# Kernel optimization log

Measured on AMD Instinct MI355X. Metric: run time of the kernel, lower is better.

## Reference

```python
import jax, jax.numpy as jnp
import numpy as np
import math

B, LC, LQ, D = 64, 1024, 128, 128


def setup_inputs() -> dict:
    key = jax.random.key(0)
    k1, k2, k3, k4, k5 = jax.random.split(key, 5)
    c_rep = jax.random.normal(k1, (B, LC, D), dtype=jnp.float32)
    q_rep = jax.random.normal(k2, (B, LQ, D), dtype=jnp.float32)
    c_mask = jax.random.randint(k3, (B, LC), 0, 2, dtype=jnp.int32)
    q_mask = jax.random.randint(k4, (B, LQ), 0, 2, dtype=jnp.int32)
    lim = math.sqrt(1.0 / D)
    w = jax.random.uniform(k5, (3 * D,), dtype=jnp.float32, minval=-lim, maxval=lim)
    return {"c_rep": c_rep, "q_rep": q_rep, "c_mask": c_mask, "q_mask": q_mask, "w": w}


def _mask_logits(t, m):
    # mask == 1 means masked (matches original: target*(1-mask) + mask*-1e30)
    return t * (1.0 - m) + m * (-1e30)


def reference(c_rep, q_rep, c_mask, q_mask, w):
    d = c_rep.shape[-1]
    w1, w2, w3 = w[:d], w[d:2 * d], w[2 * d:]
    # Trilinear similarity S[b,i,j] = <ct,w1> + <qt,w2> + <ct*qt,w3>
    # computed without materializing the [B,Lc,Lq,3D] concat tensor.
    S = (c_rep @ w1)[:, :, None] \
        + (q_rep @ w2)[:, None, :] \
        + jnp.einsum('bid,bjd->bij', c_rep * w3, q_rep)  # [B, Lc, Lq]
    qm = q_mask[:, None, :].astype(S.dtype)  # [B, 1, Lq]
    cm = c_mask[:, :, None].astype(S.dtype)  # [B, Lc, 1]
    S1 = jax.nn.softmax(_mask_logits(S, qm), axis=2)  # softmax over query dim
    S2 = jax.nn.softmax(_mask_logits(S, cm), axis=1)  # softmax over context dim
    A = jnp.einsum('bij,bjd->bid', S1, q_rep)  # [B, Lc, D]
    # B_att = S1 @ S2^T @ c_rep, associated right-first to avoid [B,Lc,Lc]
    T = jnp.einsum('bkj,bkd->bjd', S2, c_rep)  # [B, Lq, D]
    B_att = jnp.einsum('bij,bjd->bid', S1, T)  # [B, Lc, D]
    out = jnp.concatenate([c_rep, A, c_rep * A, c_rep * B_att], axis=2)  # [B, Lc, 4D]
    # dropout is identity at inference
    return out
```

## Files before the change

### kernel.cpp

```cpp
#include <hip/hip_runtime.h>
#include <hip/hip_bf16.h>
#include <cstdint>
#include <cstddef>

#define B_   64
#define LC_  1024
#define LQ_  128
#define D_   128

typedef __bf16 bf16;
typedef bf16  bf16x8 __attribute__((ext_vector_type(8)));
typedef bf16  bf16x4 __attribute__((ext_vector_type(4)));
typedef float f32x4  __attribute__((ext_vector_type(4)));

__device__ __forceinline__ f32x4 mfma16(bf16x8 a, bf16x8 b, f32x4 c) {
  return __builtin_amdgcn_mfma_f32_16x16x32_bf16(a, b, c, 0, 0, 0);
}

__global__ __launch_bounds__(256) void k0c(const float* __restrict__ c, const float* __restrict__ w,
                                           float* __restrict__ cw1, bf16* __restrict__ cw3,
                                           bf16* __restrict__ cT) {
  __shared__ float w1s[128];
  __shared__ float w3s[128];
  __shared__ bf16  ctile[128 * 132];
  const int b = blockIdx.y, ks = blockIdx.x;
  const int k0 = ks * 128;
  const int t = threadIdx.x;
  if (t < 128) { w1s[t] = w[t]; w3s[t] = w[256 + t]; }
  __syncthreads();
  {
    const int r = t >> 1, d0 = (t & 1) * 64;
    const float* crow = c + ((size_t)(b * LC_ + k0 + r) * D_ + d0);
    bf16* orow = cw3 + ((size_t)(b * LC_ + k0 + r) * D_ + d0);
    float dot = 0.f;
#pragma unroll
    for (int v = 0; v < 8; ++v) {
      const float4 f0 = ((const float4*)crow)[v * 2 + 0];
      const float4 f1 = ((const float4*)crow)[v * 2 + 1];
      const int dd = d0 + v * 8;
      dot += f0.x * w1s[dd + 0] + f0.y * w1s[dd + 1] + f0.z * w1s[dd + 2] + f0.w * w1s[dd + 3]
           + f1.x * w1s[dd + 4] + f1.y * w1s[dd + 5] + f1.z * w1s[dd + 6] + f1.w * w1s[dd + 7];
      bf16* cr = &ctile[r * 132 + dd];
      cr[0] = (bf16)f0.x; cr[1] = (bf16)f0.y; cr[2] = (bf16)f0.z; cr[3] = (bf16)f0.w;
      cr[4] = (bf16)f1.x; cr[5] = (bf16)f1.y; cr[6] = (bf16)f1.z; cr[7] = (bf16)f1.w;
      bf16x8 o;
      o[0] = (bf16)(f0.x * w3s[dd + 0]); o[1] = (bf16)(f0.y * w3s[dd + 1]);
      o[2] = (bf16)(f0.z * w3s[dd + 2]); o[3] = (bf16)(f0.w * w3s[dd + 3]);
      o[4] = (bf16)(f1.x * w3s[dd + 4]); o[5] = (bf16)(f1.y * w3s[dd + 5]);
      o[6] = (bf16)(f1.z * w3s[dd + 6]); o[7] = (bf16)(f1.w * w3s[dd + 7]);
      *(bf16x8*)(orow + v * 8) = o;
    }
    dot += __shfl_xor(dot, 1);
    if ((t & 1) == 0) cw1[b * LC_ + k0 + r] = dot;
  }
  __syncthreads();
  {
    const int d = t >> 1, kh = (t & 1) * 64;
    bf16* trow = cT + ((size_t)(b * D_ + d) * LC_ + k0 + kh);
#pragma unroll
    for (int v = 0; v < 8; ++v) {
      bf16x8 o;
#pragma unroll
      for (int e = 0; e < 8; ++e) o[e] = ctile[(kh + v * 8 + e) * 132 + d];
      *(bf16x8*)(trow + v * 8) = o;
    }
  }
}

__global__ __launch_bounds__(256) void k0q(const float* __restrict__ q, const float* __restrict__ w,
                                           float* __restrict__ qw2, bf16* __restrict__ qb,
                                           bf16* __restrict__ qT) {
  __shared__ float w2s[128];
  __shared__ bf16  qtile[128 * 132];
  const int b = blockIdx.x;
  const int t = threadIdx.x;
  if (t < 128) w2s[t] = w[128 + t];
  __syncthreads();
  {
    const int r = t >> 1, d0 = (t & 1) * 64;
    const float* qrow = q + ((size_t)(b * LQ_ + r) * D_ + d0);
    bf16* orow = qb + ((size_t)(b * LQ_ + r) * D_ + d0);
    float dot = 0.f;
#pragma unroll
    for (int v = 0; v < 8; ++v) {
      const float4 f0 = ((const float4*)qrow)[v * 2 + 0];
      const float4 f1 = ((const float4*)qrow)[v * 2 + 1];
      const int dd = d0 + v * 8;
      dot += f0.x * w2s[dd + 0] + f0.y * w2s[dd + 1] + f0.z * w2s[dd + 2] + f0.w * w2s[dd + 3]
           + f1.x * w2s[dd + 4] + f1.y * w2s[dd + 5] + f1.z * w2s[dd + 6] + f1.w * w2s[dd + 7];
      bf16x8 o;
      o[0] = (bf16)f0.x; o[1] = (bf16)f0.y; o[2] = (bf16)f0.z; o[3] = (bf16)f0.w;
      o[4] = (bf16)f1.x; o[5] = (bf16)f1.y; o[6] = (bf16)f1.z; o[7] = (bf16)f1.w;
      bf16* qr = &qtile[r * 132 + dd];
#pragma unroll
      for (int e = 0; e < 8; ++e) qr[e] = o[e];
      *(bf16x8*)(orow + v * 8) = o;
    }
    dot += __shfl_xor(dot, 1);
    if ((t & 1) == 0) qw2[b * LQ_ + r] = dot;
  }
  __syncthreads();
  {
    const int d = t >> 1, jh = (t & 1) * 64;
    bf16* trow = qT + ((size_t)(b * D_ + d) * LQ_ + jh);
#pragma unroll
    for (int v = 0; v < 8; ++v) {
      bf16x8 o;
#pragma unroll
      for (int e = 0; e < 8; ++e) o[e] = qtile[(jh + v * 8 + e) * 132 + d];
      *(bf16x8*)(trow + v * 8) = o;
    }
  }
}

__global__ __launch_bounds__(256) void k1(const float* __restrict__ cw1, const float* __restrict__ qw2,
                                          const int* __restrict__ cmask,
                                          const bf16* __restrict__ cw3, const bf16* __restrict__ cT,
                                          const bf16* __restrict__ qb, bf16* __restrict__ TT) {
  __shared__ bf16  qs[32 * 136];
  __shared__ bf16  cw3t[64 * 136];
  __shared__ bf16  cTt[128 * 72];
  __shared__ bf16  PT[32 * 72];
  __shared__ float lred[4][32];
  __shared__ float lfin[32];
  const int js = blockIdx.x, b = blockIdx.y;
  const int j0 = js * 32;
  const int t = threadIdx.x;
  const int w = t >> 6, lane = t & 63, quad = lane >> 4, l15 = lane & 15;

#pragma unroll
  for (int idx = t; idx < 512; idx += 256) {
    const int row = idx >> 4, ch = idx & 15;
    *(bf16x8*)&qs[row * 136 + ch * 8] =
        *(const bf16x8*)(qb + ((size_t)(b * LQ_ + j0 + row) * D_ + ch * 8));
  }
  const f32x4 z = {0.f, 0.f, 0.f, 0.f};
  f32x4 Tacc[2][2] = {{z, z}, {z, z}};
  float lacc0 = 0.f, lacc1 = 0.f;
  __syncthreads();

  for (int kt = 0; kt < 16; ++kt) {
    const int k0g = kt * 64;
#pragma unroll
    for (int idx = t; idx < 1024; idx += 256) {
      const int row = idx >> 4, ch = idx & 15;
      *(bf16x8*)&cw3t[row * 136 + ch * 8] =
          *(const bf16x8*)(cw3 + ((size_t)(b * LC_ + k0g + row) * D_ + ch * 8));
    }
#pragma unroll
    for (int idx = t; idx < 1024; idx += 256) {
      const int row = idx >> 3, ch = idx & 7;
      *(bf16x8*)&cTt[row * 72 + ch * 8] =
          *(const bf16x8*)(cT + ((size_t)(b * D_ + row) * LC_ + k0g + ch * 8));
    }
    __syncthreads();

    f32x4 S0 = z, S1 = z;
#pragma unroll
    for (int ks = 0; ks < 4; ++ks) {
      bf16x8 a  = *(bf16x8*)&cw3t[(w * 16 + l15) * 136 + ks * 32 + quad * 8];
      bf16x8 b0 = *(bf16x8*)&qs[l15 * 136 + ks * 32 + quad * 8];
      bf16x8 b1 = *(bf16x8*)&qs[(16 + l15) * 136 + ks * 32 + quad * 8];
      S0 = mfma16(a, b0, S0);
      S1 = mfma16(a, b1, S1);
    }
    const float qv0 = qw2[b * LQ_ + j0 + l15];
    const float qv1 = qw2[b * LQ_ + j0 + 16 + l15];
    bf16x4 pk0, pk1;
#pragma unroll
    for (int rr = 0; rr < 4; ++rr) {
      const int krow = k0g + w * 16 + quad * 4 + rr;
      const float c1 = cw1[b * LC_ + krow];
      const int   cm = cmask[b * LC_ + krow];
      const float p0 = cm ? 0.f : __expf(S0[rr] + c1 + qv0);
      const float p1 = cm ? 0.f : __expf(S1[rr] + c1 + qv1);
      lacc0 += p0; lacc1 += p1;
      pk0[rr] = (bf16)p0; pk1[rr] = (bf16)p1;
    }
    *(bf16x4*)&PT[l15 * 72 + w * 16 + quad * 4] = pk0;
    *(bf16x4*)&PT[(16 + l15) * 72 + w * 16 + quad * 4] = pk1;
    __syncthreads();

#pragma unroll
    for (int ks = 0; ks < 2; ++ks) {
      bf16x8 a0 = *(bf16x8*)&PT[l15 * 72 + ks * 32 + quad * 8];
      bf16x8 a1 = *(bf16x8*)&PT[(16 + l15) * 72 + ks * 32 + quad * 8];
      bf16x8 b0 = *(bf16x8*)&cTt[(w * 32 + l15) * 72 + ks * 32 + quad * 8];
      bf16x8 b1 = *(bf16x8*)&cTt[(w * 32 + 16 + l15) * 72 + ks * 32 + quad * 8];
      Tacc[0][0] = mfma16(a0, b0, Tacc[0][0]);
      Tacc[0][1] = mfma16(a0, b1, Tacc[0][1]);
      Tacc[1][0] = mfma16(a1, b0, Tacc[1][0]);
      Tacc[1][1] = mfma16(a1, b1, Tacc[1][1]);
    }
    __syncthreads();
  }

  lacc0 += __shfl_xor(lacc0, 16); lacc0 += __shfl_xor(lacc0, 32);
  lacc1 += __shfl_xor(lacc1, 16); lacc1 += __shfl_xor(lacc1, 32);
  if (lane < 16) { lred[w][l15] = lacc0; lred[w][16 + l15] = lacc1; }
  __syncthreads();
  if (t < 32) lfin[t] = lred[0][t] + lred[1][t] + lred[2][t] + lred[3][t];
  __syncthreads();

  bf16* TTa = cw3t;
#pragma unroll
  for (int mt = 0; mt < 2; ++mt) {
#pragma unroll
    for (int nt = 0; nt < 2; ++nt) {
      const int d = w * 32 + nt * 16 + l15;
      bf16x4 pk;
#pragma unroll
      for (int rr = 0; rr < 4; ++rr) {
        const int j = mt * 16 + quad * 4 + rr;
        pk[rr] = (bf16)(Tacc[mt][nt][rr] / lfin[j]);
      }
      *(bf16x4*)&TTa[d * 40 + mt * 16 + quad * 4] = pk;
    }
  }
  __syncthreads();
  if (t < 128) {
    bf16* dst = TT + ((size_t)(b * D_ + t) * LQ_ + j0);
#pragma unroll
    for (int v = 0; v < 4; ++v)
      *(bf16x8*)(dst + v * 8) = *(bf16x8*)&TTa[t * 40 + v * 8];
  }
}

__global__ __launch_bounds__(256) void k2(const float* __restrict__ c, const float* __restrict__ cw1,
                                          const float* __restrict__ qw2, const int* __restrict__ qmask,
                                          const bf16* __restrict__ cw3, const bf16* __restrict__ qb,
                                          const bf16* __restrict__ qT, const bf16* __restrict__ TT,
                                          float* __restrict__ out) {
  __shared__ bf16 cw3i[64 * 136];
  __shared__ bf16 qsl[32 * 136];
  __shared__ bf16 qTsl[128 * 40];
  __shared__ bf16 TTsl[128 * 40];
  __shared__ bf16 P1[64 * 40];
  const int it = blockIdx.x, b = blockIdx.y;
  const int i0 = it * 64;
  const int t = threadIdx.x;
  const int w = t >> 6, lane = t & 63, quad = lane >> 4, l15 = lane & 15;

#pragma unroll
  for (int idx = t; idx < 1024; idx += 256) {
    const int row = idx >> 4, ch = idx & 15;
    *(bf16x8*)&cw3i[row * 136 + ch * 8] =
        *(const bf16x8*)(cw3 + ((size_t)(b * LC_ + i0 + row) * D_ + ch * 8));
  }
  const f32x4 z = {0.f, 0.f, 0.f, 0.f};
  f32x4 Aacc[8], Bacc[8];
#pragma unroll
  for (int n = 0; n < 8; ++n) { Aacc[n] = z; Bacc[n] = z; }
  float lacc[4] = {0.f, 0.f, 0.f, 0.f};
  __syncthreads();

  for (int jt = 0; jt < 4; ++jt) {
    const int j0 = jt * 32;
#pragma unroll
    for (int idx = t; idx < 512; idx += 256) {
      const int row = idx >> 4, ch = idx & 15;
      *(bf16x8*)&qsl[row * 136 + ch * 8] =
          *(const bf16x8*)(qb + ((size_t)(b * LQ_ + j0 + row) * D_ + ch * 8));
    }
#pragma unroll
    for (int idx = t; idx < 512; idx += 256) {
      const int row = idx >> 2, ch = idx & 3;
      *(bf16x8*)&qTsl[row * 40 + ch * 8] =
          *(const bf16x8*)(qT + ((size_t)(b * D_ + row) * LQ_ + j0 + ch * 8));
    }
#pragma unroll
    for (int idx = t; idx < 512; idx += 256) {
      const int row = idx >> 2, ch = idx & 3;
      *(bf16x8*)&TTsl[row * 40 + ch * 8] =
          *(const bf16x8*)(TT + ((size_t)(b * D_ + row) * LQ_ + j0 + ch * 8));
    }
    __syncthreads();

    f32x4 S0 = z, S1 = z;
#pragma unroll
    for (int ks = 0; ks < 4; ++ks) {
      bf16x8 a  = *(bf16x8*)&cw3i[(w * 16 + l15) * 136 + ks * 32 + quad * 8];
      bf16x8 b0 = *(bf16x8*)&qsl[l15 * 136 + ks * 32 + quad * 8];
      bf16x8 b1 = *(bf16x8*)&qsl[(16 + l15) * 136 + ks * 32 + quad * 8];
      S0 = mfma16(a, b0, S0);
      S1 = mfma16(a, b1, S1);
    }
    const float qv0 = qw2[b * LQ_ + j0 + l15];
    const float qv1 = qw2[b * LQ_ + j0 + 16 + l15];
    const int   qm0 = qmask[b * LQ_ + j0 + l15];
    const int   qm1 = qmask[b * LQ_ + j0 + 16 + l15];
#pragma unroll
    for (int rr = 0; rr < 4; ++rr) {
      const int irow = i0 + w * 16 + quad * 4 + rr;
      const float c1 = cw1[b * LC_ + irow];
      const float p0 = qm0 ? 0.f : __expf(S0[rr] + c1 + qv0);
      const float p1 = qm1 ? 0.f : __expf(S1[rr] + c1 + qv1);
      lacc[rr] += p0 + p1;
      P1[(w * 16 + quad * 4 + rr) * 40 + l15] = (bf16)p0;
      P1[(w * 16 + quad * 4 + rr) * 40 + 16 + l15] = (bf16)p1;
    }
    __syncthreads();

    bf16x8 aP = *(bf16x8*)&P1[(w * 16 + l15) * 40 + quad * 8];
#pragma unroll
    for (int nt = 0; nt < 8; ++nt) {
      bf16x8 bq = *(bf16x8*)&qTsl[(nt * 16 + l15) * 40 + quad * 8];
      bf16x8 bt = *(bf16x8*)&TTsl[(nt * 16 + l15) * 40 + quad * 8];
      Aacc[nt] = mfma16(aP, bq, Aacc[nt]);
      Bacc[nt] = mfma16(aP, bt, Bacc[nt]);
    }
    __syncthreads();
  }

#pragma unroll
  for (int rr = 0; rr < 4; ++rr) {
    float v = lacc[rr];
    v += __shfl_xor(v, 1); v += __shfl_xor(v, 2);
    v += __shfl_xor(v, 4); v += __shfl_xor(v, 8);
    lacc[rr] = 1.f / v;
  }

#pragma unroll
  for (int nt = 0; nt < 8; ++nt) {
    const int d = nt * 16 + l15;
#pragma unroll
    for (int rr = 0; rr < 4; ++rr) {
      const int irow = i0 + w * 16 + quad * 4 + rr;
      const float Av = Aacc[nt][rr] * lacc[rr];
      const float Bv = Bacc[nt][rr] * lacc[rr];
      const float cv = c[(size_t)(b * LC_ + irow) * D_ + d];
      float* ob = out + (size_t)(b * LC_ + irow) * 512;
      ob[128 + d] = Av;
      ob[256 + d] = cv * Av;
      ob[384 + d] = cv * Bv;
    }
  }
#pragma unroll
  for (int idx = t; idx < 2048; idx += 256) {
    const int row = idx >> 5, seg = idx & 31;
    const float4 v = ((const float4*)(c + (size_t)(b * LC_ + i0 + row) * D_))[seg];
    ((float4*)(out + (size_t)(b * LC_ + i0 + row) * 512))[seg] = v;
  }
}

extern "C" void kernel_launch(void* const* d_in, const int* in_sizes, int n_in,
                              void* d_out, int out_size, void* d_ws, size_t ws_size,
                              hipStream_t stream) {
  (void)in_sizes; (void)n_in; (void)out_size; (void)ws_size;
  const float* c     = (const float*)d_in[0];
  const float* q     = (const float*)d_in[1];
  const int*   cmask = (const int*)d_in[2];
  const int*   qmask = (const int*)d_in[3];
  const float* w     = (const float*)d_in[4];
  float* out = (float*)d_out;

  char* ws = (char*)d_ws;
  float* cw1 = (float*)(ws + 0);
  float* qw2 = (float*)(ws + 262144);
  bf16*  cw3 = (bf16*)(ws + 294912);
  bf16*  cT  = (bf16*)(ws + 17072128);
  bf16*  qb  = (bf16*)(ws + 33849344);
  bf16*  qT  = (bf16*)(ws + 35946496);
  bf16*  TT  = (bf16*)(ws + 38043648);

  k0c<<<dim3(8, 64), 256, 0, stream>>>(c, w, cw1, cw3, cT);
  k0q<<<dim3(64), 256, 0, stream>>>(q, w, qw2, qb, qT);
  k1<<<dim3(4, 64), 256, 0, stream>>>(cw1, qw2, cmask, cw3, cT, qb, TT);
  k2<<<dim3(16, 64), 256, 0, stream>>>(c, cw1, qw2, qmask, cw3, qb, qT, TT, out);
}
```

Before: 266.0 us.

## Split k1 context reduction across blocks and stage k2 output through LDS

The k1 context-dimension reduction is split into two halves computed by separate blocks, doubling the grid from 256 to 512 blocks. Partial T sums and softmax denominators are written as fp32 into the output buffer as scratch, then combined and normalised by a new reduction kernel k1r. Separately, k2 now stages the A and B accumulators through shared memory so the output write becomes coalesced float4 stores of all four concatenated segments. This adds a kernel launch and extra fp32 partial traffic, and k2 gains extra syncs, in exchange for better occupancy in k1 and wider, coalesced stores in k2.

Result: faster. 246.8 us (-7.2%).

```diff
diff --git a/kernel.cpp b/kernel.cpp
--- a/kernel.cpp
+++ b/kernel.cpp
@@ -113,17 +113,19 @@
   }
 }
 
-__global__ __launch_bounds__(256) void k1(const float* __restrict__ cw1, const float* __restrict__ qw2,
-                                          const int* __restrict__ cmask,
-                                          const bf16* __restrict__ cw3, const bf16* __restrict__ cT,
-                                          const bf16* __restrict__ qb, bf16* __restrict__ TT) {
+__global__ __launch_bounds__(256) void k1p(const float* __restrict__ cw1, const float* __restrict__ qw2,
+                                           const int* __restrict__ cmask,
+                                           const bf16* __restrict__ cw3, const bf16* __restrict__ cT,
+                                           const bf16* __restrict__ qb,
+                                           float* __restrict__ Tpart, float* __restrict__ lpart) {
   __shared__ bf16  qs[32 * 136];
   __shared__ bf16  cw3t[64 * 136];
   __shared__ bf16  cTt[128 * 72];
   __shared__ bf16  PT[32 * 72];
   __shared__ float lred[4][32];
-  __shared__ float lfin[32];
-  const int js = blockIdx.x, b = blockIdx.y;
+  const int bx = blockIdx.x;
+  const int ks = bx >> 2, js = bx & 3;
+  const int b = blockIdx.y;
   const int j0 = js * 32;
   const int t = threadIdx.x;
   const int w = t >> 6, lane = t & 63, quad = lane >> 4, l15 = lane & 15;
@@ -139,8 +141,8 @@
   float lacc0 = 0.f, lacc1 = 0.f;
   __syncthreads();
 
-  for (int kt = 0; kt < 16; ++kt) {
-    const int k0g = kt * 64;
+  for (int kt = 0; kt < 8; ++kt) {
+    const int k0g = ks * 512 + kt * 64;
 #pragma unroll
     for (int idx = t; idx < 1024; idx += 256) {
       const int row = idx >> 4, ch = idx & 15;
@@ -157,10 +159,10 @@
 
     f32x4 S0 = z, S1 = z;
 #pragma unroll
-    for (int ks = 0; ks < 4; ++ks) {
-      bf16x8 a  = *(bf16x8*)&cw3t[(w * 16 + l15) * 136 + ks * 32 + quad * 8];
-      bf16x8 b0 = *(bf16x8*)&qs[l15 * 136 + ks * 32 + quad * 8];
-      bf16x8 b1 = *(bf16x8*)&qs[(16 + l15) * 136 + ks * 32 + quad * 8];
+    for (int kk = 0; kk < 4; ++kk) {
+      bf16x8 a  = *(bf16x8*)&cw3t[(w * 16 + l15) * 136 + kk * 32 + quad * 8];
+      bf16x8 b0 = *(bf16x8*)&qs[l15 * 136 + kk * 32 + quad * 8];
+      bf16x8 b1 = *(bf16x8*)&qs[(16 + l15) * 136 + kk * 32 + quad * 8];
       S0 = mfma16(a, b0, S0);
       S1 = mfma16(a, b1, S1);
     }
@@ -182,11 +184,11 @@
     __syncthreads();
 
 #pragma unroll
-    for (int ks = 0; ks < 2; ++ks) {
-      bf16x8 a0 = *(bf16x8*)&PT[l15 * 72 + ks * 32 + quad * 8];
-      bf16x8 a1 = *(bf16x8*)&PT[(16 + l15) * 72 + ks * 32 + quad * 8];
-      bf16x8 b0 = *(bf16x8*)&cTt[(w * 32 + l15) * 72 + ks * 32 + quad * 8];
-      bf16x8 b1 = *(bf16x8*)&cTt[(w * 32 + 16 + l15) * 72 + ks * 32 + quad * 8];
+    for (int kk = 0; kk < 2; ++kk) {
+      bf16x8 a0 = *(bf16x8*)&PT[l15 * 72 + kk * 32 + quad * 8];
+      bf16x8 a1 = *(bf16x8*)&PT[(16 + l15) * 72 + kk * 32 + quad * 8];
+      bf16x8 b0 = *(bf16x8*)&cTt[(w * 32 + l15) * 72 + kk * 32 + quad * 8];
+      bf16x8 b1 = *(bf16x8*)&cTt[(w * 32 + 16 + l15) * 72 + kk * 32 + quad * 8];
       Tacc[0][0] = mfma16(a0, b0, Tacc[0][0]);
       Tacc[0][1] = mfma16(a0, b1, Tacc[0][1]);
       Tacc[1][0] = mfma16(a1, b0, Tacc[1][0]);
@@ -199,31 +201,52 @@
   lacc1 += __shfl_xor(lacc1, 16); lacc1 += __shfl_xor(lacc1, 32);
   if (lane < 16) { lred[w][l15] = lacc0; lred[w][16 + l15] = lacc1; }
   __syncthreads();
-  if (t < 32) lfin[t] = lred[0][t] + lred[1][t] + lred[2][t] + lred[3][t];
-  __syncthreads();
-
-  bf16* TTa = cw3t;
-#pragma unroll
-  for (int mt = 0; mt < 2; ++mt) {
-#pragma unroll
-    for (int nt = 0; nt < 2; ++nt) {
-      const int d = w * 32 + nt * 16 + l15;
-      bf16x4 pk;
-#pragma unroll
-      for (int rr = 0; rr < 4; ++rr) {
-        const int j = mt * 16 + quad * 4 + rr;
-        pk[rr] = (bf16)(Tacc[mt][nt][rr] / lfin[j]);
-      }
-      *(bf16x4*)&TTa[d * 40 + mt * 16 + quad * 4] = pk;
-    }
-  }
-  __syncthreads();
-  if (t < 128) {
-    bf16* dst = TT + ((size_t)(b * D_ + t) * LQ_ + j0);
-#pragma unroll
-    for (int v = 0; v < 4; ++v)
-      *(bf16x8*)(dst + v * 8) = *(bf16x8*)&TTa[t * 40 + v * 8];
-  }
+  if (t < 32)
+    lpart[(size_t)(b * 2 + ks) * 128 + j0 + t] = lred[0][t] + lred[1][t] + lred[2][t] + lred[3][t];
+
+  float* tp = Tpart + ((size_t)((b * 2 + ks) * 4 + js)) * (32 * 128);
+#pragma unroll
+  for (int mt = 0; mt < 2; ++mt)
+#pragma unroll
+    for (int nt = 0; nt < 2; ++nt)
+#pragma unroll
+      for (int rr = 0; rr < 4; ++rr)
+        tp[(mt * 16 + quad * 4 + rr) * 128 + w * 32 + nt * 16 + l15] = Tacc[mt][nt][rr];
+}
+
+__global__ __launch_bounds__(256) void k1r(const float* __restrict__ Tpart,
+                                           const float* __restrict__ lpart,
+                                           bf16* __restrict__ TT) {
+  __shared__ float Tsum[32 * 132];
+  __shared__ float linv[32];
+  const int js = blockIdx.x, b = blockIdx.y;
+  const int j0 = js * 32;
+  const int t = threadIdx.x;
+  const float4* p0 = (const float4*)(Tpart + ((size_t)((b * 2 + 0) * 4 + js)) * (32 * 128));
+  const float4* p1 = (const float4*)(Tpart + ((size_t)((b * 2 + 1) * 4 + js)) * (32 * 128));
+#pragma unroll
+  for (int idx = t; idx < 1024; idx += 256) {
+    const int row = idx >> 5, seg = idx & 31;
+    const float4 v0 = p0[idx];
+    const float4 v1 = p1[idx];
+    float4 s;
+    s.x = v0.x + v1.x; s.y = v0.y + v1.y; s.z = v0.z + v1.z; s.w = v0.w + v1.w;
+    *(float4*)&Tsum[row * 132 + seg * 4] = s;
+  }
+  if (t < 32)
+    linv[t] = 1.f / (lpart[(size_t)(b * 2 + 0) * 128 + j0 + t] +
+                     lpart[(size_t)(b * 2 + 1) * 128 + j0 + t]);
+  __syncthreads();
+  const int d = t >> 1, jh = (t & 1) * 16;
+  bf16x8 o0, o1;
+#pragma unroll
+  for (int e = 0; e < 8; ++e) {
+    o0[e] = (bf16)(Tsum[(jh + e) * 132 + d] * linv[jh + e]);
+    o1[e] = (bf16)(Tsum[(jh + 8 + e) * 132 + d] * linv[jh + 8 + e]);
+  }
+  bf16* dst = TT + ((size_t)(b * D_ + d) * LQ_ + j0 + jh);
+  *(bf16x8*)dst = o0;
+  *(bf16x8*)(dst + 8) = o1;
 }
 
 __global__ __launch_bounds__(256) void k2(const float* __restrict__ c, const float* __restrict__ cw1,
@@ -231,11 +254,14 @@
                                           const bf16* __restrict__ cw3, const bf16* __restrict__ qb,
                                           const bf16* __restrict__ qT, const bf16* __restrict__ TT,
                                           float* __restrict__ out) {
-  __shared__ bf16 cw3i[64 * 136];
-  __shared__ bf16 qsl[32 * 136];
-  __shared__ bf16 qTsl[128 * 40];
-  __shared__ bf16 TTsl[128 * 40];
-  __shared__ bf16 P1[64 * 40];
+  __shared__ __align__(16) char smem[51712];
+  bf16* cw3i = (bf16*)(smem);
+  bf16* qsl  = (bf16*)(smem + 17408);
+  bf16* qTsl = (bf16*)(smem + 26112);
+  bf16* TTsl = (bf16*)(smem + 36352);
+  bf16* P1   = (bf16*)(smem + 46592);
+  float* A32 = (float*)(smem);
+  float* B32 = (float*)(smem + 16896);
   const int it = blockIdx.x, b = blockIdx.y;
   const int i0 = it * 64;
   const int t = threadIdx.x;
@@ -278,10 +304,10 @@
 
     f32x4 S0 = z, S1 = z;
 #pragma unroll
-    for (int ks = 0; ks < 4; ++ks) {
-      bf16x8 a  = *(bf16x8*)&cw3i[(w * 16 + l15) * 136 + ks * 32 + quad * 8];
-      bf16x8 b0 = *(bf16x8*)&qsl[l15 * 136 + ks * 32 + quad * 8];
-      bf16x8 b1 = *(bf16x8*)&qsl[(16 + l15) * 136 + ks * 32 + quad * 8];
+    for (int kk = 0; kk < 4; ++kk) {
+      bf16x8 a  = *(bf16x8*)&cw3i[(w * 16 + l15) * 136 + kk * 32 + quad * 8];
+      bf16x8 b0 = *(bf16x8*)&qsl[l15 * 136 + kk * 32 + quad * 8];
+      bf16x8 b1 = *(bf16x8*)&qsl[(16 + l15) * 136 + kk * 32 + quad * 8];
       S0 = mfma16(a, b0, S0);
       S1 = mfma16(a, b1, S1);
     }
@@ -321,25 +347,34 @@
   }
 
 #pragma unroll
-  for (int nt = 0; nt < 8; ++nt) {
-    const int d = nt * 16 + l15;
-#pragma unroll
-    for (int rr = 0; rr < 4; ++rr) {
-      const int irow = i0 + w * 16 + quad * 4 + rr;
-      const float Av = Aacc[nt][rr] * lacc[rr];
-      const float Bv = Bacc[nt][rr] * lacc[rr];
-      const float cv = c[(size_t)(b * LC_ + irow) * D_ + d];
-      float* ob = out + (size_t)(b * LC_ + irow) * 512;
-      ob[128 + d] = Av;
-      ob[256 + d] = cv * Av;
-      ob[384 + d] = cv * Bv;
-    }
-  }
-#pragma unroll
-  for (int idx = t; idx < 2048; idx += 256) {
-    const int row = idx >> 5, seg = idx & 31;
-    const float4 v = ((const float4*)(c + (size_t)(b * LC_ + i0 + row) * D_))[seg];
-    ((float4*)(out + (size_t)(b * LC_ + i0 + row) * 512))[seg] = v;
+  for (int h = 0; h < 2; ++h) {
+    if ((w >> 1) == h) {
+      const int lrow0 = (w & 1) * 16 + quad * 4;
+#pragma unroll
+      for (int nt = 0; nt < 8; ++nt)
+#pragma unroll
+        for (int rr = 0; rr < 4; ++rr) {
+          A32[(lrow0 + rr) * 132 + nt * 16 + l15] = Aacc[nt][rr] * lacc[rr];
+          B32[(lrow0 + rr) * 132 + nt * 16 + l15] = Bacc[nt][rr] * lacc[rr];
+        }
+    }
+    __syncthreads();
+#pragma unroll
+    for (int idx = t; idx < 1024; idx += 256) {
+      const int lrow = idx >> 5, seg = idx & 31;
+      const size_t grow = (size_t)(b * LC_ + i0 + h * 32 + lrow);
+      const float4 c4 = ((const float4*)(c + grow * D_))[seg];
+      const float4 a4 = *(float4*)&A32[lrow * 132 + seg * 4];
+      const float4 b4 = *(float4*)&B32[lrow * 132 + seg * 4];
+      float4* ob = (float4*)(out + grow * 512);
+      ob[seg] = c4;
+      ob[32 + seg] = a4;
+      float4 ca; ca.x = c4.x * a4.x; ca.y = c4.y * a4.y; ca.z = c4.z * a4.z; ca.w = c4.w * a4.w;
+      ob[64 + seg] = ca;
+      float4 cb; cb.x = c4.x * b4.x; cb.y = c4.y * b4.y; cb.z = c4.z * b4.z; cb.w = c4.w * b4.w;
+      ob[96 + seg] = cb;
+    }
+    __syncthreads();
   }
 }
 
@@ -363,8 +398,12 @@
   bf16*  qT  = (bf16*)(ws + 35946496);
   bf16*  TT  = (bf16*)(ws + 38043648);
 
+  float* Tpart = out;
+  float* lpart = out + 2097152;
+
   k0c<<<dim3(8, 64), 256, 0, stream>>>(c, w, cw1, cw3, cT);
   k0q<<<dim3(64), 256, 0, stream>>>(q, w, qw2, qb, qT);
-  k1<<<dim3(4, 64), 256, 0, stream>>>(cw1, qw2, cmask, cw3, cT, qb, TT);
+  k1p<<<dim3(8, 64), 256, 0, stream>>>(cw1, qw2, cmask, cw3, cT, qb, Tpart, lpart);
+  k1r<<<dim3(4, 64), 256, 0, stream>>>(Tpart, lpart, TT);
   k2<<<dim3(16, 64), 256, 0, stream>>>(c, cw1, qw2, qmask, cw3, qb, qT, TT, out);
 }
```
